# Kernel tuning notes

Hardware: AMD Instinct MI355X
Metric: run time of the kernel (lower is better)

## Reference

```python
import jax, jax.numpy as jnp
import numpy as np

B, H, W, DIM = 16, 64, 64, 256
EXPAND = 2
D_INNER = DIM * EXPAND      # 512
HID = D_INNER // 2          # 256 per GRU direction


def setup_inputs() -> dict:
    ks = jax.random.split(jax.random.key(0), 10)
    g = lambda i, shape, s=0.05: jax.random.normal(ks[i], shape, dtype=jnp.float32) * s
    return {
        "x": jax.random.normal(ks[0], (B, H, W, DIM), dtype=jnp.float32),
        "ln_gamma": jnp.ones((DIM,), jnp.float32),
        "ln_beta": jnp.zeros((DIM,), jnp.float32),
        "mlp_w1": g(1, (32, 4), 0.3),
        "mlp_b1": jnp.zeros((32,), jnp.float32),
        "mlp_w2": g(2, (4, 32), 0.3),
        "mlp_b2": jnp.zeros((4,), jnp.float32),
        "in_w": g(3, (D_INNER, DIM)),
        "in_b": jnp.zeros((D_INNER,), jnp.float32),
        "gru_wih_f": g(4, (3 * HID, D_INNER)),
        "gru_whh_f": g(5, (3 * HID, HID)),
        "gru_bih_f": jnp.zeros((3 * HID,), jnp.float32),
        "gru_bhh_f": jnp.zeros((3 * HID,), jnp.float32),
        "gru_wih_b": g(6, (3 * HID, D_INNER)),
        "gru_whh_b": g(7, (3 * HID, HID)),
        "gru_bih_b": jnp.zeros((3 * HID,), jnp.float32),
        "gru_bhh_b": jnp.zeros((3 * HID,), jnp.float32),
        "out_w": g(8, (DIM, D_INNER)),
        "out_b": jnp.zeros((DIM,), jnp.float32),
    }


def _resize_linear_axis(x, out_size, axis):
    """torch F.interpolate(mode='bilinear', align_corners=False) along one axis
    (the other axis has scale 1 -> identity, so 1-D resize is exact)."""
    in_size = x.shape[axis]
    scale = in_size / out_size
    src = (jnp.arange(out_size, dtype=jnp.float32) + 0.5) * scale - 0.5
    src = jnp.clip(src, 0.0, in_size - 1)
    i0 = jnp.floor(src).astype(jnp.int32)
    i1 = jnp.minimum(i0 + 1, in_size - 1)
    w = (src - i0.astype(jnp.float32))
    x0 = jnp.take(x, i0, axis=axis)
    x1 = jnp.take(x, i1, axis=axis)
    shape = [1] * x.ndim
    shape[axis] = out_size
    w = w.reshape(shape)
    return x0 * (1.0 - w) + x1 * w


def _avgpool3_mean(g):
    """F.avg_pool2d(g, 3, stride=1, padding=1) (count_include_pad=True), then
    spatial mean -> [B, 1]."""
    s = jax.lax.reduce_window(g, 0.0, jax.lax.add, (1, 1, 3, 3), (1, 1, 1, 1),
                              [(0, 0), (0, 0), (1, 1), (1, 1)])
    return (s / 9.0).mean(axis=(2, 3))


def _gru_dir(xp, whh, bhh, reverse):
    """One GRU direction. xp: [B, L, 3h] precomputed input-side gates."""
    hid = whh.shape[1]
    h0 = jnp.zeros((xp.shape[0], hid), xp.dtype)

    def step(h, xt):
        gh = h @ whh.T + bhh
        xr, xz, xn = jnp.split(xt, 3, axis=-1)
        hr, hz, hn = jnp.split(gh, 3, axis=-1)
        r = jax.nn.sigmoid(xr + hr)
        z = jax.nn.sigmoid(xz + hz)
        n = jnp.tanh(xn + r * hn)
        h_new = (1.0 - z) * n + z * h
        return h_new, h_new

    _, ys = jax.lax.scan(step, h0, jnp.swapaxes(xp, 0, 1), reverse=reverse)
    return jnp.swapaxes(ys, 0, 1)  # [B, L, h], ys[t] aligned with input t


def _forward(x, ln_gamma, ln_beta, mlp_w1, mlp_b1, mlp_w2, mlp_b2,
             in_w, in_b, gru_wih_f, gru_whh_f, gru_bih_f, gru_bhh_f,
             gru_wih_b, gru_whh_b, gru_bih_b, gru_bhh_b, out_w, out_b):
    Bx, Hx, Wx, C = x.shape
    # LayerNorm over channels
    mu = x.mean(-1, keepdims=True)
    var = ((x - mu) ** 2).mean(-1, keepdims=True)
    xn = (x - mu) / jnp.sqrt(var + 1e-5) * ln_gamma + ln_beta

    # --- GradientDirectionSelector ---
    gray = xn.mean(-1)[:, None]                                   # [B,1,H,W]
    gp = jnp.pad(gray, ((0, 0), (0, 0), (1, 1), (1, 1)), mode="reflect")
    grad_h = jnp.abs(gp[:, :, :, 2:] - gp[:, :, :, :-2])          # [B,1,H+2,W]
    grad_v = jnp.abs(gp[:, :, 2:, :] - gp[:, :, :-2, :])          # [B,1,H,W+2]
    grad_h = _resize_linear_axis(grad_h, Hx, axis=2)              # [B,1,H,W]
    grad_v = _resize_linear_axis(grad_v, Wx, axis=3)              # [B,1,H,W]
    grad_d = (grad_h + grad_v) * 0.5
    grad_a = jnp.abs(grad_h - grad_v)
    scores = jnp.concatenate(
        [_avgpool3_mean(g) for g in (grad_h, grad_v, grad_d, grad_a)], axis=1)  # [B,4]
    h1 = jax.nn.relu(scores @ mlp_w1.T + mlp_b1)
    logits = h1 @ mlp_w2.T + mlp_b2
    probs = jax.nn.softmax(logits, axis=-1)
    idx = jnp.argmax(probs, axis=-1)  # topk=1 indices, [B]

    # --- direction-routed scan (dir 1 -> vertical transpose; 0/2/3 -> row-major) ---
    seq_h = xn.reshape(Bx, Hx * Wx, C)
    seq_v = jnp.swapaxes(xn, 1, 2).reshape(Bx, Hx * Wx, C)
    seq = jnp.where((idx == 1)[:, None, None], seq_v, seq_h)      # [B,L,C]

    # --- FastSequenceBlock: in_proj -> biGRU -> out_proj ---
    z = seq @ in_w.T + in_b                                       # [B,L,d_inner]
    yf = _gru_dir(z @ gru_wih_f.T + gru_bih_f, gru_whh_f, gru_bhh_f, False)
    yb = _gru_dir(z @ gru_wih_b.T + gru_bih_b, gru_whh_b, gru_bhh_b, True)
    y = jnp.concatenate([yf, yb], axis=-1) @ out_w.T + out_b      # [B,L,C]

    # unscan (row-major reshape, as in the original) + residual
    return x + y.reshape(Bx, Hx, Wx, C)


def reference(x, ln_gamma, ln_beta, mlp_w1, mlp_b1, mlp_w2, mlp_b2,
              in_w, in_b, gru_wih_f, gru_whh_f, gru_bih_f, gru_bhh_f,
              gru_wih_b, gru_whh_b, gru_bih_b, gru_bhh_b, out_w, out_b):
    return _forward(x, ln_gamma, ln_beta, mlp_w1, mlp_b1, mlp_w2, mlp_b2,
                    in_w, in_b, gru_wih_f, gru_whh_f, gru_bih_f, gru_bhh_f,
                    gru_wih_b, gru_whh_b, gru_bih_b, gru_bhh_b, out_w, out_b)
```

## Files before the change

kernel.cpp:

```cpp
#include <hip/hip_runtime.h>


#define L_   4096
#define CH   32
#define NCH  128

typedef __attribute__((ext_vector_type(8))) _Float16 half8;
typedef __attribute__((ext_vector_type(4))) float f32x4;

__device__ __forceinline__ unsigned short f2h(float f) {
  _Float16 h = (_Float16)f;
  return __builtin_bit_cast(unsigned short, h);
}
__device__ __forceinline__ float h2f(unsigned short u) {
  return (float)__builtin_bit_cast(_Float16, u);
}
__device__ __forceinline__ float sigm(float x) {
  return __builtin_amdgcn_rcpf(1.f + __expf(-x));
}
__device__ __forceinline__ float tanhf_(float x) {
  return 1.f - 2.f * __builtin_amdgcn_rcpf(1.f + __expf(2.f * x));
}

__global__ __launch_bounds__(256) void k_f2h(const float* __restrict__ in,
                                             unsigned short* __restrict__ out,
                                             int n) {
  int i = blockIdx.x * 256 + threadIdx.x;
  if (i < n) out[i] = f2h(in[i]);
}

__global__ __launch_bounds__(256) void k_wcomb(const float* __restrict__ wih_f,
                                               const float* __restrict__ wih_b,
                                               const float* __restrict__ in_w,
                                               unsigned short* __restrict__ wcomb) {
  const int n = blockIdx.x;
  const float* wrow = (n < 768) ? (wih_f + (long)n * 512)
                                : (wih_b + (long)(n - 768) * 512);
  const int k = threadIdx.x;
  float acc = 0.f;
  for (int j = 0; j < 512; ++j) acc += wrow[j] * in_w[j * 256 + k];
  wcomb[(long)n * 256 + k] = f2h(acc);
}

__global__ __launch_bounds__(256) void k_bcomb(const float* __restrict__ wih_f,
                                               const float* __restrict__ wih_b,
                                               const float* __restrict__ in_b,
                                               const float* __restrict__ bih_f,
                                               const float* __restrict__ bih_b,
                                               float* __restrict__ bcomb) {
  int n = blockIdx.x * 256 + threadIdx.x;
  if (n >= 1536) return;
  const float* wrow = (n < 768) ? (wih_f + (long)n * 512)
                                : (wih_b + (long)(n - 768) * 512);
  float acc = (n < 768) ? bih_f[n] : bih_b[n - 768];
  for (int j = 0; j < 512; ++j) acc += wrow[j] * in_b[j];
  bcomb[n] = acc;
}

__global__ __launch_bounds__(256) void k_ln(const float* __restrict__ x,
                                            const float* __restrict__ gamma,
                                            const float* __restrict__ beta,
                                            unsigned short* __restrict__ xn,
                                            float* __restrict__ gray) {
  const int lane = threadIdx.x & 63;
  const long pix = (long)blockIdx.x * 4 + (threadIdx.x >> 6);
  const float4 v = *(const float4*)(x + pix * 256 + lane * 4);
  float s = v.x + v.y + v.z + v.w;
  float s2 = v.x * v.x + v.y * v.y + v.z * v.z + v.w * v.w;
#pragma unroll
  for (int off = 32; off > 0; off >>= 1) {
    s += __shfl_xor(s, off, 64);
    s2 += __shfl_xor(s2, off, 64);
  }
  const float mu = s * (1.f / 256.f);
  const float var = fmaxf(s2 * (1.f / 256.f) - mu * mu, 0.f);
  const float rstd = rsqrtf(var + 1e-5f);
  const float4 gm = *(const float4*)(gamma + lane * 4);
  const float4 bt = *(const float4*)(beta + lane * 4);
  float o0 = (v.x - mu) * rstd * gm.x + bt.x;
  float o1 = (v.y - mu) * rstd * gm.y + bt.y;
  float o2 = (v.z - mu) * rstd * gm.z + bt.z;
  float o3 = (v.w - mu) * rstd * gm.w + bt.w;
  ushort4 o;
  o.x = f2h(o0); o.y = f2h(o1); o.z = f2h(o2); o.w = f2h(o3);
  *(ushort4*)(xn + pix * 256 + lane * 4) = o;
  float gs = o0 + o1 + o2 + o3;
#pragma unroll
  for (int off = 32; off > 0; off >>= 1) gs += __shfl_xor(gs, off, 64);
  if (lane == 0) gray[pix] = gs * (1.f / 256.f);
}

__device__ __forceinline__ int refl64(int m) {
  return m < 0 ? -m : (m > 63 ? 126 - m : m);
}

__global__ __launch_bounds__(256) void k_sel(const float* __restrict__ gray,
                                             const float* __restrict__ w1,
                                             const float* __restrict__ b1,
                                             const float* __restrict__ w2,
                                             const float* __restrict__ b2,
                                             int* __restrict__ flag) {
  __shared__ float g[64][65];
  __shared__ float part[4][4];
  const int b = blockIdx.x;
  const int tid = threadIdx.x;
  for (int r = 0; r < 16; ++r) {
    int p = tid + 256 * r;
    g[p >> 6][p & 63] = gray[(long)b * 4096 + p];
  }
  __syncthreads();
  const float S = 66.f / 64.f;
  float sh = 0.f, sv = 0.f, sd = 0.f, sa = 0.f;
  for (int rr = 0; rr < 16; ++rr) {
    int p = tid + 256 * rr;
    int h = p >> 6, w = p & 63;
    float srci = (h + 0.5f) * S - 0.5f;
    int i0 = (int)srci;
    float ai = srci - (float)i0;
    int i1 = i0 + 1; if (i1 > 65) i1 = 65;
    int r0 = refl64(i0 - 1), r1 = refl64(i1 - 1);
    int wl = w ? (w - 1) : 1;
    int wr2 = (w == 63) ? 62 : (w + 1);
    float GH0 = fabsf(g[r0][wr2] - g[r0][wl]);
    float GH1 = fabsf(g[r1][wr2] - g[r1][wl]);
    float ghr = GH0 + ai * (GH1 - GH0);
    float srcj = (w + 0.5f) * S - 0.5f;
    int j0 = (int)srcj;
    float aj = srcj - (float)j0;
    int j1 = j0 + 1; if (j1 > 65) j1 = 65;
    int c0 = refl64(j0 - 1), c1 = refl64(j1 - 1);
    int hu = h ? (h - 1) : 1;
    int hd = (h == 63) ? 62 : (h + 1);
    float GV0 = fabsf(g[hd][c0] - g[hu][c0]);
    float GV1 = fabsf(g[hd][c1] - g[hu][c1]);
    float gvr = GV0 + aj * (GV1 - GV0);
    float wt = ((h == 0 || h == 63) ? 2.f : 3.f) *
               ((w == 0 || w == 63) ? 2.f : 3.f);
    sh += wt * ghr;
    sv += wt * gvr;
    sd += wt * 0.5f * (ghr + gvr);
    sa += wt * fabsf(ghr - gvr);
  }
#pragma unroll
  for (int off = 32; off > 0; off >>= 1) {
    sh += __shfl_xor(sh, off, 64);
    sv += __shfl_xor(sv, off, 64);
    sd += __shfl_xor(sd, off, 64);
    sa += __shfl_xor(sa, off, 64);
  }
  if ((tid & 63) == 0) {
    part[tid >> 6][0] = sh; part[tid >> 6][1] = sv;
    part[tid >> 6][2] = sd; part[tid >> 6][3] = sa;
  }
  __syncthreads();
  if (tid == 0) {
    float sc[4];
    for (int k = 0; k < 4; ++k)
      sc[k] = (part[0][k] + part[1][k] + part[2][k] + part[3][k]) * (1.f / 36864.f);
    float logits[4];
    for (int k = 0; k < 4; ++k) logits[k] = b2[k];
    for (int j = 0; j < 32; ++j) {
      float hj = b1[j];
      for (int i = 0; i < 4; ++i) hj += sc[i] * w1[j * 4 + i];
      hj = fmaxf(hj, 0.f);
      for (int k = 0; k < 4; ++k) logits[k] += hj * w2[k * 32 + j];
    }
    int idx = 0;
    float best = logits[0];
    for (int k = 1; k < 4; ++k)
      if (logits[k] > best) { best = logits[k]; idx = k; }
    flag[b] = (idx == 1) ? 1 : 0;
  }
}

__global__ __launch_bounds__(256) void k_gemm(const unsigned short* __restrict__ A,
                                              const unsigned short* __restrict__ Bw,
                                              const float* __restrict__ bias,
                                              const float* __restrict__ resid,
                                              float* __restrict__ out,
                                              int K, int N) {
  __shared__ unsigned short Al[128][40];
  __shared__ unsigned short Bl[128][40];
  const int tid = threadIdx.x;
  const long m0 = (long)blockIdx.x * 128;
  const int n0 = blockIdx.y * 128;
  const int rA = tid >> 2;
  const int cp = (tid & 3) * 8;

  const unsigned short* a0p = A + (m0 + rA) * K + cp;
  const unsigned short* a1p = A + (m0 + rA + 64) * K + cp;
  const unsigned short* b0p = Bw + (long)(n0 + rA) * K + cp;
  const unsigned short* b1p = Bw + (long)(n0 + rA + 64) * K + cp;

  const int wv = tid >> 6, lane = tid & 63;
  const int wm = (wv >> 1) * 64, wn = (wv & 1) * 64;
  const int fr = lane & 15, fq = lane >> 4;

  const f32x4 zero4 = {0.f, 0.f, 0.f, 0.f};
  f32x4 acc[4][4];
#pragma unroll
  for (int i = 0; i < 4; ++i)
#pragma unroll
    for (int j = 0; j < 4; ++j) acc[i][j] = zero4;

  for (int k0 = 0; k0 < K; k0 += 32) {
    half8 va0 = *(const half8*)(a0p + k0);
    half8 va1 = *(const half8*)(a1p + k0);
    half8 vb0 = *(const half8*)(b0p + k0);
    half8 vb1 = *(const half8*)(b1p + k0);
    __syncthreads();
    *(half8*)&Al[rA][cp] = va0;
    *(half8*)&Al[rA + 64][cp] = va1;
    *(half8*)&Bl[rA][cp] = vb0;
    *(half8*)&Bl[rA + 64][cp] = vb1;
    __syncthreads();
    half8 af[4], bf[4];
#pragma unroll
    for (int i = 0; i < 4; ++i) af[i] = *(const half8*)&Al[wm + i * 16 + fr][fq * 8];
#pragma unroll
    for (int j = 0; j < 4; ++j) bf[j] = *(const half8*)&Bl[wn + j * 16 + fr][fq * 8];
#pragma unroll
    for (int i = 0; i < 4; ++i)
#pragma unroll
      for (int j = 0; j < 4; ++j)
        acc[i][j] = __builtin_amdgcn_mfma_f32_16x16x32_f16(af[i], bf[j], acc[i][j], 0, 0, 0);
  }

#pragma unroll
  for (int j = 0; j < 4; ++j) {
    const int col = n0 + wn + j * 16 + fr;
    const float bv = bias[col];
#pragma unroll
    for (int i = 0; i < 4; ++i) {
      const long mbase = m0 + wm + i * 16 + fq * 4;
#pragma unroll
      for (int r = 0; r < 4; ++r) {
        const long m = mbase + r;
        out[m * N + col] = acc[i][j][r] + bv + resid[m * N + col];
      }
    }
  }
}

__global__ __launch_bounds__(512, 2) void k_scan(
    const unsigned short* __restrict__ xn,
    const unsigned short* __restrict__ wcomb,
    const float* __restrict__ bcomb,
    const unsigned short* __restrict__ whhf,
    const unsigned short* __restrict__ whhb,
    const float* __restrict__ bhhf,
    const float* __restrict__ bhhb,
    const int* __restrict__ flag,
    unsigned short* __restrict__ ycat) {
  const int dir = blockIdx.x & 1;
  const int b = blockIdx.x >> 1;
  const unsigned short* whh = dir ? whhb : whhf;
  const float* bhh = dir ? bhhb : bhhf;
  const unsigned short* wcd = wcomb + (long)dir * (768 * 256);
  const float* bcd = bcomb + dir * 768;
  const int tid = threadIdx.x;
  const int wv = tid >> 6;
  const int lane = tid & 63;
  const int fr = lane & 15;
  const int fq = lane >> 4;
  const int fb = flag[b];

  half8 wf[6][8];
#pragma unroll
  for (int j = 0; j < 6; ++j) {
    const unsigned short* wrow =
        whh + (long)(((wv + 8 * j) << 4) + fr) * 256 + fq * 8;
#pragma unroll
    for (int s = 0; s < 8; ++s) wf[j][s] = *(const half8*)(wrow + s * 32);
  }

  __shared__ unsigned short xplds[CH][768];
  __shared__ unsigned short hlds[256];
  __shared__ float ghlds[768];

  float br = 0.f, bz = 0.f, bnh = 0.f, bcn = 0.f, hreg = 0.f;
  if (tid < 256) {
    hlds[tid] = 0;
    br = bhh[tid] + bcd[tid];
    bz = bhh[256 + tid] + bcd[256 + tid];
    bnh = bhh[512 + tid];
    bcn = bcd[512 + tid];
  }
  __syncthreads();

  const long xnb = (long)b * 4096;
  unsigned short* yb = ycat + (long)b * (L_ * 512) + dir * 256;

  const f32x4 zero4 = {0.f, 0.f, 0.f, 0.f};
  const half8 zero8h = {0, 0, 0, 0, 0, 0, 0, 0};

  for (int c = 0; c < NCH; ++c) {
    const int cc = dir ? (NCH - 1 - c) : c;
    const int t0 = cc * CH;

    const unsigned short* arow0;
    const unsigned short* arow1;
    {
      int t = t0 + fr;
      int p = fb ? (((t & 63) << 6) | (t >> 6)) : t;
      arow0 = xn + (xnb + p) * 256 + fq * 8;
      t = t0 + 16 + fr;
      p = fb ? (((t & 63) << 6) | (t >> 6)) : t;
      arow1 = xn + (xnb + p) * 256 + fq * 8;
    }
#pragma unroll
    for (int hf = 0; hf < 2; ++hf) {
      f32x4 acc0[3], acc1[3];
#pragma unroll
      for (int j = 0; j < 3; ++j) { acc0[j] = zero4; acc1[j] = zero4; }
#pragma unroll
      for (int s = 0; s < 8; ++s) {
        half8 a0 = *(const half8*)(arow0 + s * 32);
        half8 a1 = *(const half8*)(arow1 + s * 32);
#pragma unroll
        for (int j = 0; j < 3; ++j) {
          const int n = wv * 96 + hf * 48 + j * 16 + fr;
          half8 bfr = *(const half8*)(wcd + (long)n * 256 + s * 32 + fq * 8);
          acc0[j] = __builtin_amdgcn_mfma_f32_16x16x32_f16(a0, bfr, acc0[j], 0, 0, 0);
          acc1[j] = __builtin_amdgcn_mfma_f32_16x16x32_f16(a1, bfr, acc1[j], 0, 0, 0);
        }
      }
#pragma unroll
      for (int j = 0; j < 3; ++j) {
        const int n = wv * 96 + hf * 48 + j * 16 + fr;
#pragma unroll
        for (int r = 0; r < 4; ++r) {
          xplds[fq * 4 + r][n] = f2h(acc0[j][r]);
          xplds[16 + fq * 4 + r][n] = f2h(acc1[j][r]);
        }
      }
    }
    __syncthreads();

    for (int lt = 0; lt < CH; ++lt) {
      const int ts = dir ? (CH - 1 - lt) : lt;
      float xr = 0.f, xz = 0.f, xnv = 0.f;
      if (tid < 256) {
        xr = h2f(xplds[ts][tid]);
        xz = h2f(xplds[ts][256 + tid]);
        xnv = h2f(xplds[ts][512 + tid]);
      }
      f32x4 acc[6];
#pragma unroll
      for (int s = 0; s < 8; ++s) {
        half8 a = zero8h;
        if (fr == 0) a = *(const half8*)&hlds[s * 32 + fq * 8];
#pragma unroll
        for (int j = 0; j < 6; ++j) {
          f32x4 cin = (s == 0) ? zero4 : acc[j];
          acc[j] = __builtin_amdgcn_mfma_f32_16x16x32_f16(a, wf[j][s], cin, 0, 0, 0);
        }
      }
      if (lane < 16) {
#pragma unroll
        for (int j = 0; j < 6; ++j)
          ghlds[((wv + 8 * j) << 4) + lane] = acc[j][0];
      }
      __syncthreads();
      if (tid < 256) {
        float r = sigm(xr + ghlds[tid] + br);
        float z = sigm(xz + ghlds[256 + tid] + bz);
        float n = tanhf_(xnv + bcn + r * (ghlds[512 + tid] + bnh));
        float hn = n + z * (hreg - n);
        hreg = hn;
        unsigned short hb = f2h(hn);
        hlds[tid] = hb;
        yb[(long)(t0 + ts) * 512 + tid] = hb;
      }
      __syncthreads();
    }
  }
}

extern "C" void kernel_launch(void* const* d_in, const int* in_sizes, int n_in,
                              void* d_out, int out_size, void* d_ws, size_t ws_size,
                              hipStream_t stream) {
  (void)in_sizes; (void)n_in; (void)out_size; (void)ws_size;
  const float* x     = (const float*)d_in[0];
  const float* lng   = (const float*)d_in[1];
  const float* lnb   = (const float*)d_in[2];
  const float* w1    = (const float*)d_in[3];
  const float* b1    = (const float*)d_in[4];
  const float* w2    = (const float*)d_in[5];
  const float* b2    = (const float*)d_in[6];
  const float* in_w  = (const float*)d_in[7];
  const float* in_b  = (const float*)d_in[8];
  const float* wih_f = (const float*)d_in[9];
  const float* whh_f = (const float*)d_in[10];
  const float* bih_f = (const float*)d_in[11];
  const float* bhh_f = (const float*)d_in[12];
  const float* wih_b = (const float*)d_in[13];
  const float* whh_b = (const float*)d_in[14];
  const float* bih_b = (const float*)d_in[15];
  const float* bhh_b = (const float*)d_in[16];
  const float* out_w = (const float*)d_in[17];
  const float* out_b = (const float*)d_in[18];

  char* ws = (char*)d_ws;
  unsigned short* xn    = (unsigned short*)(ws + 0);
  float*          gray  = (float*)(ws + 33554432);
  int*            flag  = (int*)(ws + 33816576);
  unsigned short* whhf16 = (unsigned short*)(ws + 33816832);
  unsigned short* whhb16 = (unsigned short*)(ws + 34210048);
  unsigned short* outw16 = (unsigned short*)(ws + 34603264);
  unsigned short* wcomb  = (unsigned short*)(ws + 34865408);
  float*          bcomb  = (float*)(ws + 35651840);
  unsigned short* ycat   = (unsigned short*)(ws + 35658240);

  k_f2h<<<768, 256, 0, stream>>>(whh_f, whhf16, 196608);
  k_f2h<<<768, 256, 0, stream>>>(whh_b, whhb16, 196608);
  k_f2h<<<512, 256, 0, stream>>>(out_w, outw16, 131072);
  k_wcomb<<<1536, 256, 0, stream>>>(wih_f, wih_b, in_w, wcomb);
  k_bcomb<<<6, 256, 0, stream>>>(wih_f, wih_b, in_b, bih_f, bih_b, bcomb);
  k_ln<<<16384, 256, 0, stream>>>(x, lng, lnb, xn, gray);
  k_sel<<<16, 256, 0, stream>>>(gray, w1, b1, w2, b2, flag);
  k_scan<<<32, 512, 0, stream>>>(xn, wcomb, bcomb, whhf16, whhb16,
                                 bhh_f, bhh_b, flag, ycat);
  dim3 gout(512, 2);
  k_gemm<<<gout, 256, 0, stream>>>(ycat, outw16, out_b, x, (float*)d_out, 512, 256);
}
```

Baseline: 7.130 ms.

## Permute recurrent weights so each wave owns whole units, dropping a per-step barrier

A new prep kernel permutes W_hh rows so each wave's six MFMA output tiles cover the r, z and n gates of the same 32 hidden units. That lets each wave apply the GRU gate math directly from its accumulators, without staging gate sums through shared memory. With a double-buffered hidden state this removes one of the two __syncthreads per timestep. Per-step global stores of h are replaced by a shared staging buffer flushed as vectorized half8 stores at the start of the next chunk. The trade-off is that gate math now runs on only 16 lanes per wave, two units each, and there is extra shared memory plus a flush phase per chunk.

Measured after the change: 7.382 ms. 1.04x slower.

```diff
diff --git a/kernel.cpp b/kernel.cpp
--- a/kernel.cpp
+++ b/kernel.cpp
@@ -27,6 +27,22 @@
                                              int n) {
   int i = blockIdx.x * 256 + threadIdx.x;
   if (i < n) out[i] = f2h(in[i]);
+}
+
+__global__ __launch_bounds__(256) void k_whhP(const float* __restrict__ whh_f,
+                                              const float* __restrict__ whh_b,
+                                              unsigned short* __restrict__ whhP) {
+  const int x = blockIdx.x;
+  const int dir = x >= 768;
+  const int p = dir ? (x - 768) : x;
+  const int w = p / 96;
+  const int r = p - w * 96;
+  const int j = r >> 4;
+  const int l = r & 15;
+  const int g = j >> 1;
+  const int u = w * 32 + (j & 1) * 16 + l;
+  const float* src = (dir ? whh_b : whh_f) + (long)(g * 256 + u) * 256;
+  whhP[(long)x * 256 + threadIdx.x] = f2h(src[threadIdx.x]);
 }
 
 __global__ __launch_bounds__(256) void k_wcomb(const float* __restrict__ wih_f,
@@ -246,15 +262,14 @@
     const unsigned short* __restrict__ xn,
     const unsigned short* __restrict__ wcomb,
     const float* __restrict__ bcomb,
-    const unsigned short* __restrict__ whhf,
-    const unsigned short* __restrict__ whhb,
+    const unsigned short* __restrict__ whhP,
     const float* __restrict__ bhhf,
     const float* __restrict__ bhhb,
     const int* __restrict__ flag,
     unsigned short* __restrict__ ycat) {
   const int dir = blockIdx.x & 1;
   const int b = blockIdx.x >> 1;
-  const unsigned short* whh = dir ? whhb : whhf;
+  const unsigned short* whh = whhP + (long)dir * (768 * 256);
   const float* bhh = dir ? bhhb : bhhf;
   const unsigned short* wcd = wcomb + (long)dir * (768 * 256);
   const float* bcd = bcomb + dir * 768;
@@ -269,23 +284,30 @@
 #pragma unroll
   for (int j = 0; j < 6; ++j) {
     const unsigned short* wrow =
-        whh + (long)(((wv + 8 * j) << 4) + fr) * 256 + fq * 8;
+        whh + (long)((wv * 6 + j) * 16 + fr) * 256 + fq * 8;
 #pragma unroll
     for (int s = 0; s < 8; ++s) wf[j][s] = *(const half8*)(wrow + s * 32);
   }
 
   __shared__ unsigned short xplds[CH][768];
-  __shared__ unsigned short hlds[256];
-  __shared__ float ghlds[768];
-
-  float br = 0.f, bz = 0.f, bnh = 0.f, bcn = 0.f, hreg = 0.f;
-  if (tid < 256) {
-    hlds[tid] = 0;
-    br = bhh[tid] + bcd[tid];
-    bz = bhh[256 + tid] + bcd[256 + tid];
-    bnh = bhh[512 + tid];
-    bcn = bcd[512 + tid];
-  }
+  __shared__ unsigned short ylds[CH][256];
+  __shared__ unsigned short hbuf[2][256];
+
+  const int u0 = wv * 32 + fr;
+  float Br0 = 0.f, Br1 = 0.f, Bz0 = 0.f, Bz1 = 0.f;
+  float Bnh0 = 0.f, Bnh1 = 0.f, Bcn0 = 0.f, Bcn1 = 0.f;
+  float h0 = 0.f, h1 = 0.f;
+  if (lane < 16) {
+    Br0 = bhh[u0] + bcd[u0];
+    Br1 = bhh[u0 + 16] + bcd[u0 + 16];
+    Bz0 = bhh[256 + u0] + bcd[256 + u0];
+    Bz1 = bhh[256 + u0 + 16] + bcd[256 + u0 + 16];
+    Bnh0 = bhh[512 + u0];
+    Bnh1 = bhh[512 + u0 + 16];
+    Bcn0 = bcd[512 + u0];
+    Bcn1 = bcd[512 + u0 + 16];
+  }
+  if (tid < 256) hbuf[0][tid] = 0;
   __syncthreads();
 
   const long xnb = (long)b * 4096;
@@ -293,10 +315,23 @@
 
   const f32x4 zero4 = {0.f, 0.f, 0.f, 0.f};
   const half8 zero8h = {0, 0, 0, 0, 0, 0, 0, 0};
+  int pb = 0;
 
   for (int c = 0; c < NCH; ++c) {
     const int cc = dir ? (NCH - 1 - c) : c;
     const int t0 = cc * CH;
+
+    if (c > 0) {
+      const int pt0 = (dir ? (NCH - c) : (c - 1)) * CH;
+#pragma unroll
+      for (int k = 0; k < 2; ++k) {
+        const int idx = tid * 2 + k;
+        const int ts = idx >> 5;
+        const int cl = (idx & 31) * 8;
+        half8 v = *(const half8*)&ylds[ts][cl];
+        *(half8*)(yb + (long)(pt0 + ts) * 512 + cl) = v;
+      }
+    }
 
     const unsigned short* arow0;
     const unsigned short* arow1;
@@ -339,17 +374,20 @@
 
     for (int lt = 0; lt < CH; ++lt) {
       const int ts = dir ? (CH - 1 - lt) : lt;
-      float xr = 0.f, xz = 0.f, xnv = 0.f;
-      if (tid < 256) {
-        xr = h2f(xplds[ts][tid]);
-        xz = h2f(xplds[ts][256 + tid]);
-        xnv = h2f(xplds[ts][512 + tid]);
+      float xr0 = 0.f, xr1 = 0.f, xz0 = 0.f, xz1 = 0.f, xn0 = 0.f, xn1 = 0.f;
+      if (lane < 16) {
+        xr0 = h2f(xplds[ts][u0]);
+        xr1 = h2f(xplds[ts][u0 + 16]);
+        xz0 = h2f(xplds[ts][256 + u0]);
+        xz1 = h2f(xplds[ts][256 + u0 + 16]);
+        xn0 = h2f(xplds[ts][512 + u0]);
+        xn1 = h2f(xplds[ts][512 + u0 + 16]);
       }
       f32x4 acc[6];
 #pragma unroll
       for (int s = 0; s < 8; ++s) {
         half8 a = zero8h;
-        if (fr == 0) a = *(const half8*)&hlds[s * 32 + fq * 8];
+        if (fr == 0) a = *(const half8*)&hbuf[pb][s * 32 + fq * 8];
 #pragma unroll
         for (int j = 0; j < 6; ++j) {
           f32x4 cin = (s == 0) ? zero4 : acc[j];
@@ -357,22 +395,34 @@
         }
       }
       if (lane < 16) {
-#pragma unroll
-        for (int j = 0; j < 6; ++j)
-          ghlds[((wv + 8 * j) << 4) + lane] = acc[j][0];
-      }
+        float r0 = sigm(xr0 + acc[0][0] + Br0);
+        float r1 = sigm(xr1 + acc[1][0] + Br1);
+        float z0 = sigm(xz0 + acc[2][0] + Bz0);
+        float z1 = sigm(xz1 + acc[3][0] + Bz1);
+        float n0 = tanhf_(xn0 + Bcn0 + r0 * (acc[4][0] + Bnh0));
+        float n1 = tanhf_(xn1 + Bcn1 + r1 * (acc[5][0] + Bnh1));
+        h0 = n0 + z0 * (h0 - n0);
+        h1 = n1 + z1 * (h1 - n1);
+        unsigned short hb0 = f2h(h0);
+        unsigned short hb1 = f2h(h1);
+        hbuf[pb ^ 1][u0] = hb0;
+        hbuf[pb ^ 1][u0 + 16] = hb1;
+        ylds[ts][u0] = hb0;
+        ylds[ts][u0 + 16] = hb1;
+      }
+      pb ^= 1;
       __syncthreads();
-      if (tid < 256) {
-        float r = sigm(xr + ghlds[tid] + br);
-        float z = sigm(xz + ghlds[256 + tid] + bz);
-        float n = tanhf_(xnv + bcn + r * (ghlds[512 + tid] + bnh));
-        float hn = n + z * (hreg - n);
-        hreg = hn;
-        unsigned short hb = f2h(hn);
-        hlds[tid] = hb;
-        yb[(long)(t0 + ts) * 512 + tid] = hb;
-      }
-      __syncthreads();
+    }
+  }
+  {
+    const int pt0 = (dir ? 0 : (NCH - 1)) * CH;
+#pragma unroll
+    for (int k = 0; k < 2; ++k) {
+      const int idx = tid * 2 + k;
+      const int ts = idx >> 5;
+      const int cl = (idx & 31) * 8;
+      half8 v = *(const half8*)&ylds[ts][cl];
+      *(half8*)(yb + (long)(pt0 + ts) * 512 + cl) = v;
     }
   }
 }
@@ -402,24 +452,22 @@
   const float* out_b = (const float*)d_in[18];
 
   char* ws = (char*)d_ws;
-  unsigned short* xn    = (unsigned short*)(ws + 0);
-  float*          gray  = (float*)(ws + 33554432);
-  int*            flag  = (int*)(ws + 33816576);
-  unsigned short* whhf16 = (unsigned short*)(ws + 33816832);
-  unsigned short* whhb16 = (unsigned short*)(ws + 34210048);
+  unsigned short* xn     = (unsigned short*)(ws + 0);
+  float*          gray   = (float*)(ws + 33554432);
+  int*            flag   = (int*)(ws + 33816576);
+  unsigned short* whhP   = (unsigned short*)(ws + 33816832);
   unsigned short* outw16 = (unsigned short*)(ws + 34603264);
   unsigned short* wcomb  = (unsigned short*)(ws + 34865408);
   float*          bcomb  = (float*)(ws + 35651840);
   unsigned short* ycat   = (unsigned short*)(ws + 35658240);
 
-  k_f2h<<<768, 256, 0, stream>>>(whh_f, whhf16, 196608);
-  k_f2h<<<768, 256, 0, stream>>>(whh_b, whhb16, 196608);
+  k_whhP<<<1536, 256, 0, stream>>>(whh_f, whh_b, whhP);
   k_f2h<<<512, 256, 0, stream>>>(out_w, outw16, 131072);
   k_wcomb<<<1536, 256, 0, stream>>>(wih_f, wih_b, in_w, wcomb);
   k_bcomb<<<6, 256, 0, stream>>>(wih_f, wih_b, in_b, bih_f, bih_b, bcomb);
   k_ln<<<16384, 256, 0, stream>>>(x, lng, lnb, xn, gray);
   k_sel<<<16, 256, 0, stream>>>(gray, w1, b1, w2, b2, flag);
-  k_scan<<<32, 512, 0, stream>>>(xn, wcomb, bcomb, whhf16, whhb16,
+  k_scan<<<32, 512, 0, stream>>>(xn, wcomb, bcomb, whhP,
                                  bhh_f, bhh_b, flag, ycat);
   dim3 gout(512, 2);
   k_gemm<<<gout, 256, 0, stream>>>(ycat, outw16, out_b, x, (float*)d_out, 512, 256);
```
